# Optimization experiments

Measured on AMD Instinct MI355X. Metric: run time of the kernel, lower is better.

The kernel has to match this reference:

```python
import jax, jax.numpy as jnp
import numpy as np
from math import pi

# Layer dims for num_inputs=0, width=64, depth=5, num_outputs=3
CHANNELS = [4, 64, 64, 64, 64, 3]

def _splits():
    biases, weights, idx = [], [], 0
    for l in range(len(CHANNELS) - 1):
        nci, nco = CHANNELS[l], CHANNELS[l + 1]
        biases.append((idx, idx + nco)); idx += nco
        weights.append((idx, idx + nci * nco)); idx += nci * nco
    return biases, weights, idx

BIASES, WEIGHTS, NUM_PARAMS = _splits()  # NUM_PARAMS == 12995


def _get_coords(h, w, ds):
    """Faithful port of _get_coords, including the original's bug where the
    y-channels reuse the normalized x coordinate vector (requires h == w)."""
    scale = 7.0 / 8.0
    x = jnp.arange(w, dtype=jnp.float32)
    y = jnp.arange(h, dtype=jnp.float32)
    x_c = (jnp.remainder(x, ds) / ds)
    y_c = (jnp.remainder(y, ds) / ds)
    x_c = x_c / (x_c.max() / scale)          # x_cos == x_sin in original
    y_cn = x_c / (y_c.max() / scale)          # bug: built from x_c
    xcos = jnp.cos(2.0 * pi * x_c)
    xsin = jnp.sin(2.0 * pi * x_c)
    ycos = jnp.cos(2.0 * pi * y_cn)           # length w, laid out along h (h==w)
    ysin = jnp.sin(2.0 * pi * y_cn)
    row = lambda v: jnp.broadcast_to(v[None, :], (h, w))
    col = lambda v: jnp.broadcast_to(v[:, None], (h, w))
    return jnp.stack([row(xcos), row(xsin), col(ycos), col(ysin)], axis=0)  # (4,h,w)


def setup_inputs() -> dict:
    key = jax.random.key(0)
    k1, k2 = jax.random.split(key)
    highres = jax.random.normal(k1, (2, 4, 512, 512), dtype=jnp.float32)
    lr_params = jax.random.normal(k2, (2, NUM_PARAMS, 64, 64), dtype=jnp.float32)
    return {"highres": highres, "lr_params": lr_params}


def reference(highres, lr_params):
    bs, _, h, w = highres.shape
    h_lr, w_lr = lr_params.shape[2], lr_params.shape[3]
    k = h // h_lr  # tile size

    coords = _get_coords(h, w, k)                       # (4, h, w)
    pe = jnp.broadcast_to(coords[None], (bs, 4, h, w))  # highres is overwritten by PE

    # unfold into (bs, h_lr, w_lr, k*k, 4) tiles
    tiles = pe.reshape(bs, 4, h_lr, k, w_lr, k)
    tiles = tiles.transpose(0, 2, 4, 3, 5, 1).reshape(bs, h_lr, w_lr, k * k, 4)

    out = tiles
    num_layers = len(CHANNELS) - 1
    for idx in range(num_layers):
        nci, nco = CHANNELS[idx], CHANNELS[idx + 1]
        b0, b1 = BIASES[idx]
        w0, w1 = WEIGHTS[idx]
        w_ = lr_params[:, w0:w1].transpose(0, 2, 3, 1).reshape(bs, h_lr, w_lr, nci, nco)
        b_ = lr_params[:, b0:b1].transpose(0, 2, 3, 1)[:, :, :, None, :]  # (bs,h_lr,w_lr,1,nco)
        out = jnp.einsum('bhwpi,bhwio->bhwpo', out, w_) + b_
        if idx < num_layers - 1:
            out = jnp.where(out >= 0, out, 0.01 * out)  # leaky_relu(0.01)
        else:
            out = jnp.tanh(out)

    out = out.reshape(bs, h_lr, w_lr, k, k, CHANNELS[-1])
    out = out.transpose(0, 5, 1, 3, 2, 4).reshape(bs, CHANNELS[-1], h, w)
    return out
```

## Files before the change

### kernel.cpp

```cpp
#include <hip/hip_runtime.h>
#include <math.h>


static constexpr int PLANE = 4096;
static constexpr int NPAR  = 12995;
static constexpr int WROW  = 164;
static constexpr int AHI   = 8192;

__device__ __forceinline__ float leaky(float v) { return fmaxf(v, 0.01f * v); }

__device__ __forceinline__ constexpr float cx(int k) {
  constexpr float R = 0.70710678118654752f;
  const float t[8] = {1.f, R, 0.f, -R, -1.f, -R, 0.f, R};
  return t[k];
}
__device__ __forceinline__ constexpr float sx(int k) {
  constexpr float R = 0.70710678118654752f;
  const float t[8] = {0.f, R, 1.f, R, 0.f, -R, -1.f, -R};
  return t[k];
}

__global__ __launch_bounds__(256, 1) void pqn(const float* __restrict__ lr,
                                              float* __restrict__ out) {
  __shared__ alignas(16) float A[2 * AHI];
  __shared__ alignas(16) float WB[4][4 * WROW];

  const int tid = threadIdx.x;
  const int j   = tid & 3;
  const int pg  = (tid >> 2) & 7;
  const int cob = tid >> 5;

  const int n  = blockIdx.x;
  const int e2 = (n >> 3) & 3;
  const int P  = (n & 7) | ((n >> 5) << 3);
  const int jg = ((P & 3) << 2) | e2;
  const int i  = (P >> 2) & 63;
  const int b  = (P >> 8) & 1;

  const float* __restrict__ wb =
      lr + (size_t)b * NPAR * PLANE + (size_t)(i * 64 + jg * 4);
  const float* __restrict__ pt = wb + j;

  float fyc, fys;
  sincosf(0.78539816339744830962f * pg, &fys, &fyc);

  const int abase = pg * 16 + j * 4;
  const int wrow  = j * WROW;
  const int sq    = tid >> 7;
  const int sc    = tid & 127;

  auto gaddr = [&](int g) -> size_t {
    return 384 + (size_t)(g >> 3) * 4160 + (size_t)(g & 7) * 512;
  };

  float4 paA, paB, pbA, pbB;
  {
    const size_t cb = gaddr(0);
    paA = *(const float4*)(wb + (cb + tid) * PLANE);
    paB = *(const float4*)(wb + (cb + 256 + tid) * PLANE);
  }
  float l0b[8], l0w[32], bb[8];
#pragma unroll
  for (int m = 0; m < 8; ++m) l0b[m] = pt[(size_t)(cob * 8 + m) * PLANE];
#pragma unroll
  for (int f = 0; f < 4; ++f)
#pragma unroll
    for (int m = 0; m < 8; ++m)
      l0w[f * 8 + m] = pt[(size_t)(64 + f * 64 + cob * 8 + m) * PLANE];
#pragma unroll
  for (int m = 0; m < 8; ++m) bb[m] = pt[(size_t)(320 + cob * 8 + m) * PLANE];

#pragma unroll
  for (int col = 0; col < 8; ++col) {
    float t[8];
#pragma unroll
    for (int k = 0; k < 8; ++k) {
      float v = l0b[col];
      v = fmaf(cx(k), l0w[col], v);
      v = fmaf(sx(k), l0w[8 + col], v);
      v = fmaf(fyc,  l0w[16 + col], v);
      v = fmaf(fys,  l0w[24 + col], v);
      t[k] = leaky(v);
    }
    float4 v0, v1;
    v0.x = t[0]; v0.y = t[1]; v0.z = t[2]; v0.w = t[3];
    v1.x = t[4]; v1.y = t[5]; v1.z = t[6]; v1.w = t[7];
    *(float4*)&A[(cob * 8 + col) * 128 + abase]       = v0;
    *(float4*)&A[(cob * 8 + col) * 128 + abase + AHI] = v1;
  }
#pragma unroll
  for (int jj = 0; jj < 4; ++jj) {
    WB[sq][jj * WROW + sc]     = ((const float*)&paA)[jj];
    WB[2 + sq][jj * WROW + sc] = ((const float*)&paB)[jj];
  }
  {
    size_t cb = gaddr(1);
    paA = *(const float4*)(wb + (cb + tid) * PLANE);
    paB = *(const float4*)(wb + (cb + 256 + tid) * PLANE);
    cb = gaddr(2);
    pbA = *(const float4*)(wb + (cb + tid) * PLANE);
    pbB = *(const float4*)(wb + (cb + 256 + tid) * PLANE);
  }
  asm volatile("s_waitcnt lgkmcnt(0)" ::: "memory");
  __builtin_amdgcn_s_barrier();
  __builtin_amdgcn_sched_barrier(0);

  float y[64];
#pragma unroll
  for (int m = 0; m < 64; ++m) y[m] = 0.f;

  auto cgrp = [&](int g) {
    const int r0 = (g & 7) * 8;
#pragma unroll
    for (int q = 0; q < 4; ++q) {
      const float* Wt = WB[q];
#pragma unroll
      for (int cl = 0; cl < 2; ++cl) {
        const int ci = r0 + q * 2 + cl;
        const float4 a0 = *(const float4*)&A[ci * 128 + abase];
        const float4 a1 = *(const float4*)&A[ci * 128 + abase + AHI];
        const float4 w0 = *(const float4*)&Wt[wrow + cl * 64 + cob * 8];
        const float4 w1 = *(const float4*)&Wt[wrow + cl * 64 + cob * 8 + 4];
        const float av[8] = {a0.x, a0.y, a0.z, a0.w, a1.x, a1.y, a1.z, a1.w};
        const float wv[8] = {w0.x, w0.y, w0.z, w0.w, w1.x, w1.y, w1.z, w1.w};
#pragma unroll
        for (int col = 0; col < 8; ++col)
#pragma unroll
          for (int k = 0; k < 8; ++k)
            y[col * 8 + k] = fmaf(av[k], wv[col], y[col * 8 + k]);
      }
    }
    asm volatile("s_waitcnt lgkmcnt(0)" ::: "memory");
    __builtin_amdgcn_s_barrier();
    __builtin_amdgcn_sched_barrier(0);
  };
  auto flush = [&](int l) {
#pragma unroll
    for (int col = 0; col < 8; ++col) {
      float4 v0, v1;
      v0.x = leaky(y[col * 8 + 0] + bb[col]);
      v0.y = leaky(y[col * 8 + 1] + bb[col]);
      v0.z = leaky(y[col * 8 + 2] + bb[col]);
      v0.w = leaky(y[col * 8 + 3] + bb[col]);
      v1.x = leaky(y[col * 8 + 4] + bb[col]);
      v1.y = leaky(y[col * 8 + 5] + bb[col]);
      v1.z = leaky(y[col * 8 + 6] + bb[col]);
      v1.w = leaky(y[col * 8 + 7] + bb[col]);
      *(float4*)&A[(cob * 8 + col) * 128 + abase]       = v0;
      *(float4*)&A[(cob * 8 + col) * 128 + abase + AHI] = v1;
    }
#pragma unroll
    for (int m = 0; m < 64; ++m) y[m] = 0.f;
    if (l < 2) {
#pragma unroll
      for (int m = 0; m < 8; ++m)
        bb[m] = pt[(size_t)(320 + (l + 1) * 4160 + cob * 8 + m) * PLANE];
    }
  };

#pragma unroll 1
  for (int u = 0; u < 12; ++u) {
    const int g0 = u * 2;
    cgrp(g0);
#pragma unroll
    for (int jj = 0; jj < 4; ++jj) {
      WB[sq][jj * WROW + sc]     = ((const float*)&paA)[jj];
      WB[2 + sq][jj * WROW + sc] = ((const float*)&paB)[jj];
    }
    if (g0 + 3 < 24) {
      const size_t cb = gaddr(g0 + 3);
      paA = *(const float4*)(wb + (cb + tid) * PLANE);
      paB = *(const float4*)(wb + (cb + 256 + tid) * PLANE);
    }
    asm volatile("s_waitcnt lgkmcnt(0)" ::: "memory");
    __builtin_amdgcn_s_barrier();
    __builtin_amdgcn_sched_barrier(0);

    const int g1 = g0 + 1;
    cgrp(g1);
    if ((g1 & 7) == 7) flush(g1 >> 3);
    if (g1 + 1 < 24) {
#pragma unroll
      for (int jj = 0; jj < 4; ++jj) {
        WB[sq][jj * WROW + sc]     = ((const float*)&pbA)[jj];
        WB[2 + sq][jj * WROW + sc] = ((const float*)&pbB)[jj];
      }
    }
    if (g1 + 3 < 24) {
      const size_t cb = gaddr(g1 + 3);
      pbA = *(const float4*)(wb + (cb + tid) * PLANE);
      pbB = *(const float4*)(wb + (cb + 256 + tid) * PLANE);
    }
    asm volatile("s_waitcnt lgkmcnt(0)" ::: "memory");
    __builtin_amdgcn_s_barrier();
    __builtin_amdgcn_sched_barrier(0);
  }

  float po[24];
#pragma unroll
  for (int m = 0; m < 24; ++m) po[m] = 0.f;
#pragma unroll
  for (int cl = 0; cl < 8; ++cl) {
    const int ci = cob * 8 + cl;
    const float4 a0 = *(const float4*)&A[ci * 128 + abase];
    const float4 a1 = *(const float4*)&A[ci * 128 + abase + AHI];
#pragma unroll
    for (int o = 0; o < 3; ++o) {
      const float w = pt[(size_t)(12803 + ci * 3 + o) * PLANE];
      po[o * 8 + 0] = fmaf(a0.x, w, po[o * 8 + 0]);
      po[o * 8 + 1] = fmaf(a0.y, w, po[o * 8 + 1]);
      po[o * 8 + 2] = fmaf(a0.z, w, po[o * 8 + 2]);
      po[o * 8 + 3] = fmaf(a0.w, w, po[o * 8 + 3]);
      po[o * 8 + 4] = fmaf(a1.x, w, po[o * 8 + 4]);
      po[o * 8 + 5] = fmaf(a1.y, w, po[o * 8 + 5]);
      po[o * 8 + 6] = fmaf(a1.z, w, po[o * 8 + 6]);
      po[o * 8 + 7] = fmaf(a1.w, w, po[o * 8 + 7]);
    }
  }
  asm volatile("s_waitcnt lgkmcnt(0)" ::: "memory");
  __builtin_amdgcn_s_barrier();
  float* R = A;
#pragma unroll
  for (int m = 0; m < 24; m += 4)
    *(float4*)&R[tid * 28 + m] = *(float4*)&po[m];
  asm volatile("s_waitcnt lgkmcnt(0)" ::: "memory");
  __builtin_amdgcn_s_barrier();
  __builtin_amdgcn_sched_barrier(0);

  if (cob == 0) {
#pragma unroll
    for (int o = 0; o < 3; ++o) {
      const float bias = pt[(size_t)(12800 + o) * PLANE];
      float s[8];
#pragma unroll
      for (int k = 0; k < 8; ++k) s[k] = bias;
#pragma unroll
      for (int cb = 0; cb < 8; ++cb) {
#pragma unroll
        for (int k = 0; k < 8; ++k)
          s[k] += R[(cb * 32 + tid) * 28 + o * 8 + k];
      }
      float4 v0, v1;
      v0.x = tanhf(s[0]); v0.y = tanhf(s[1]); v0.z = tanhf(s[2]); v0.w = tanhf(s[3]);
      v1.x = tanhf(s[4]); v1.y = tanhf(s[5]); v1.z = tanhf(s[6]); v1.w = tanhf(s[7]);
      float* op = out + (size_t)b * 786432 + (size_t)o * 262144 +
                  (size_t)(i * 8 + pg) * 512 + (size_t)((jg * 4 + j) * 8);
      *(float4*)op = v0;
      *(float4*)(op + 4) = v1;
    }
  }
}

extern "C" void kernel_launch(void* const* d_in, const int* in_sizes, int n_in,
                              void* d_out, int out_size, void* d_ws, size_t ws_size,
                              hipStream_t stream) {
  (void)in_sizes; (void)n_in; (void)d_ws; (void)ws_size; (void)out_size;
  const float* lr = (const float*)d_in[1];
  float* out = (float*)d_out;
  hipLaunchKernelGGL(pqn, dim3(2048), dim3(256), 0, stream, lr, out);
}
```

Measured before the change: 250.8 us.

## Double-buffer weight tiles in LDS with XOR swizzle, halving barriers per group

Replaces the single padded weight buffer with two XOR-swizzled 2048-float LDS buffers, so the next group's weights are written into one buffer while compute reads the other. This removes the extra barrier that followed each compute group, leaving one barrier per group plus one after each layer flush. The XOR swizzle replaces row padding as the way to avoid bank conflicts. In exchange the LDS footprint grows slightly and the indexing gets more complex, and correctness depends on the buffer alternation lining up with the prefetch registers.

```diff
diff --git a/kernel.cpp b/kernel.cpp
--- a/kernel.cpp
+++ b/kernel.cpp
@@ -4,7 +4,6 @@
 
 static constexpr int PLANE = 4096;
 static constexpr int NPAR  = 12995;
-static constexpr int WROW  = 164;
 static constexpr int AHI   = 8192;
 
 __device__ __forceinline__ float leaky(float v) { return fmaxf(v, 0.01f * v); }
@@ -23,7 +22,7 @@
 __global__ __launch_bounds__(256, 1) void pqn(const float* __restrict__ lr,
                                               float* __restrict__ out) {
   __shared__ alignas(16) float A[2 * AHI];
-  __shared__ alignas(16) float WB[4][4 * WROW];
+  __shared__ alignas(16) float WB[2][2048];
 
   const int tid = threadIdx.x;
   const int j   = tid & 3;
@@ -45,7 +44,8 @@
   sincosf(0.78539816339744830962f * pg, &fys, &fyc);
 
   const int abase = pg * 16 + j * 4;
-  const int wrow  = j * WROW;
+  const int swz   = j * 4;
+  const int wr0   = (cob * 8) ^ swz;
   const int sq    = tid >> 7;
   const int sc    = tid & 127;
 
@@ -90,8 +90,8 @@
   }
 #pragma unroll
   for (int jj = 0; jj < 4; ++jj) {
-    WB[sq][jj * WROW + sc]     = ((const float*)&paA)[jj];
-    WB[2 + sq][jj * WROW + sc] = ((const float*)&paB)[jj];
+    WB[0][sq * 512       + jj * 128 + (sc ^ (jj * 4))] = ((const float*)&paA)[jj];
+    WB[0][(2 + sq) * 512 + jj * 128 + (sc ^ (jj * 4))] = ((const float*)&paB)[jj];
   }
   {
     size_t cb = gaddr(1);
@@ -109,18 +109,18 @@
 #pragma unroll
   for (int m = 0; m < 64; ++m) y[m] = 0.f;
 
-  auto cgrp = [&](int g) {
+  auto cgrp = [&](int g, int h) {
     const int r0 = (g & 7) * 8;
 #pragma unroll
     for (int q = 0; q < 4; ++q) {
-      const float* Wt = WB[q];
+      const float* Wt = &WB[h][q * 512 + j * 128];
 #pragma unroll
       for (int cl = 0; cl < 2; ++cl) {
         const int ci = r0 + q * 2 + cl;
         const float4 a0 = *(const float4*)&A[ci * 128 + abase];
         const float4 a1 = *(const float4*)&A[ci * 128 + abase + AHI];
-        const float4 w0 = *(const float4*)&Wt[wrow + cl * 64 + cob * 8];
-        const float4 w1 = *(const float4*)&Wt[wrow + cl * 64 + cob * 8 + 4];
+        const float4 w0 = *(const float4*)&Wt[(cl * 64) + wr0];
+        const float4 w1 = *(const float4*)&Wt[((cl * 64 + cob * 8 + 4) ^ swz)];
         const float av[8] = {a0.x, a0.y, a0.z, a0.w, a1.x, a1.y, a1.z, a1.w};
         const float wv[8] = {w0.x, w0.y, w0.z, w0.w, w1.x, w1.y, w1.z, w1.w};
 #pragma unroll
@@ -130,9 +130,6 @@
             y[col * 8 + k] = fmaf(av[k], wv[col], y[col * 8 + k]);
       }
     }
-    asm volatile("s_waitcnt lgkmcnt(0)" ::: "memory");
-    __builtin_amdgcn_s_barrier();
-    __builtin_amdgcn_sched_barrier(0);
   };
   auto flush = [&](int l) {
 #pragma unroll
@@ -161,29 +158,27 @@
 #pragma unroll 1
   for (int u = 0; u < 12; ++u) {
     const int g0 = u * 2;
-    cgrp(g0);
 #pragma unroll
     for (int jj = 0; jj < 4; ++jj) {
-      WB[sq][jj * WROW + sc]     = ((const float*)&paA)[jj];
-      WB[2 + sq][jj * WROW + sc] = ((const float*)&paB)[jj];
+      WB[1][sq * 512       + jj * 128 + (sc ^ (jj * 4))] = ((const float*)&paA)[jj];
+      WB[1][(2 + sq) * 512 + jj * 128 + (sc ^ (jj * 4))] = ((const float*)&paB)[jj];
     }
     if (g0 + 3 < 24) {
       const size_t cb = gaddr(g0 + 3);
       paA = *(const float4*)(wb + (cb + tid) * PLANE);
       paB = *(const float4*)(wb + (cb + 256 + tid) * PLANE);
     }
+    cgrp(g0, 0);
     asm volatile("s_waitcnt lgkmcnt(0)" ::: "memory");
     __builtin_amdgcn_s_barrier();
     __builtin_amdgcn_sched_barrier(0);
 
     const int g1 = g0 + 1;
-    cgrp(g1);
-    if ((g1 & 7) == 7) flush(g1 >> 3);
     if (g1 + 1 < 24) {
 #pragma unroll
       for (int jj = 0; jj < 4; ++jj) {
-        WB[sq][jj * WROW + sc]     = ((const float*)&pbA)[jj];
-        WB[2 + sq][jj * WROW + sc] = ((const float*)&pbB)[jj];
+        WB[0][sq * 512       + jj * 128 + (sc ^ (jj * 4))] = ((const float*)&pbA)[jj];
+        WB[0][(2 + sq) * 512 + jj * 128 + (sc ^ (jj * 4))] = ((const float*)&pbB)[jj];
       }
     }
     if (g1 + 3 < 24) {
@@ -191,9 +186,16 @@
       pbA = *(const float4*)(wb + (cb + tid) * PLANE);
       pbB = *(const float4*)(wb + (cb + 256 + tid) * PLANE);
     }
+    cgrp(g1, 1);
     asm volatile("s_waitcnt lgkmcnt(0)" ::: "memory");
     __builtin_amdgcn_s_barrier();
     __builtin_amdgcn_sched_barrier(0);
+    if ((g1 & 7) == 7) {
+      flush(g1 >> 3);
+      asm volatile("s_waitcnt lgkmcnt(0)" ::: "memory");
+      __builtin_amdgcn_s_barrier();
+      __builtin_amdgcn_sched_barrier(0);
+    }
   }
 
   float po[24];
```

Result: no change. 249.2 us (-0.7%).
